# Optimization experiments

Hardware: AMD Instinct MI355X
Metric: run time of the kernel (lower is better)

The kernel has to match this reference:

```python
import jax, jax.numpy as jnp
import numpy as np

B, S, D = 4, 2048, 1024
E, H, K = 32, 128, 2


def setup_inputs() -> dict:
    key = jax.random.key(0)
    k1, k2, k3, k4 = jax.random.split(key, 4)
    scale_d = 1.0 / np.sqrt(D)
    scale_h = 1.0 / np.sqrt(H)
    return {
        "x": jax.random.normal(k1, (B, S, D), dtype=jnp.float32),
        "w_sel": jax.random.normal(k2, (E, D), dtype=jnp.float32) * scale_d,      # router Linear weight [E, D]
        "w_keys": jax.random.normal(k3, (E, D, H), dtype=jnp.float32) * scale_d,  # per-expert up-proj
        "w_values": jax.random.normal(k4, (E, H, D), dtype=jnp.float32) * scale_h, # per-expert down-proj
        "k": K,
    }


def reference(x, w_sel, w_keys, w_values, k):
    # Router: sigmoid gating + top-k expert selection per token.
    sel = jax.nn.sigmoid(jnp.einsum('bsd,ed->bse', x, w_sel))      # [B,S,E]
    sel_val, sel_idx = jax.lax.top_k(sel, k)                       # [B,S,k]
    n_exp = w_sel.shape[0]
    # Dense gate matrix: gate[b,s,e] = sum of sel_val over heads routed to e
    # (top_k indices are distinct, so this matches the per-head accumulation).
    gate = jnp.sum(jax.nn.one_hot(sel_idx, n_exp, dtype=x.dtype) * sel_val[..., None], axis=-2)  # [B,S,E]
    # Expert up-projection + ReLU for all experts (dense equivalent of the
    # per-token gathered keys[expert_idx](token); unselected experts are
    # zeroed by the gate so the math is identical).
    scores = jax.nn.relu(jnp.einsum('bsd,edh->bseh', x, w_keys))   # [B,S,E,H]
    weighted = scores * gate[..., None]                            # [B,S,E,H]
    out = jnp.einsum('bseh,ehd->bsd', weighted, w_values)          # [B,S,D]
    return out
```

## Files before the change

### kernel.cpp

```cpp
#include <hip/hip_runtime.h>
#include <cstdint>
#include <cstddef>

#define NTOK 8192
#define DIM  1024
#define NEXP 32
#define NH   128
#define TT   64
#define FTILES 16
#define BK   128
#define RT   32
#define LCAP 1024

typedef __attribute__((ext_vector_type(8))) short short8;
typedef __attribute__((ext_vector_type(4))) float float4_;

static __device__ __forceinline__ unsigned short f2bf(float f) {
  unsigned u = __float_as_uint(f);
  return (unsigned short)((u + 0x7fffu + ((u >> 16) & 1u)) >> 16);
}
static __device__ __forceinline__ float bf2f(unsigned short h) {
  return __uint_as_float(((unsigned)h) << 16);
}
static __device__ __forceinline__ void gload_lds16(const unsigned short* g,
                                                   unsigned short* l) {
  __builtin_amdgcn_global_load_lds(
      (const __attribute__((address_space(1))) unsigned int*)(const void*)g,
      (__attribute__((address_space(3))) unsigned int*)(void*)l, 16, 0, 0);
}

__global__ __launch_bounds__(256) void prep_kernel(
    const float* __restrict__ w_keys, const float* __restrict__ w_values,
    const float* __restrict__ x,
    unsigned short* __restrict__ wk_t, unsigned short* __restrict__ wv_t,
    unsigned short* __restrict__ xbf, int* __restrict__ counts)
{
  __shared__ float tile[32][33];
  const int bid = blockIdx.x;
  const int tid = threadIdx.x;
  if (bid == 0 && tid < NEXP) counts[tid] = 0;

  if (bid < 8192) {
    const float* src; unsigned short* dst; int R, C, lb;
    if (bid < 4096) { src = w_keys;   dst = wk_t; R = DIM; C = NH;  lb = bid; }
    else            { src = w_values; dst = wv_t; R = NH;  C = DIM; lb = bid - 4096; }
    const int e  = lb >> 7;
    const int t  = lb & 127;
    const int tpc = C >> 5;
    const int r0 = (t / tpc) * 32;
    const int c0 = (t % tpc) * 32;
    const float* s = src + (size_t)e * R * C;
    unsigned short* d = dst + (size_t)e * R * C;

    const int i = tid >> 3;
    const int j = (tid & 7) * 4;
    float4 v = *(const float4*)(s + (size_t)(r0 + i) * C + c0 + j);
    tile[i][j] = v.x; tile[i][j + 1] = v.y; tile[i][j + 2] = v.z; tile[i][j + 3] = v.w;
    __syncthreads();
    unsigned lo = (unsigned)f2bf(tile[j + 0][i]) | ((unsigned)f2bf(tile[j + 1][i]) << 16);
    unsigned hi = (unsigned)f2bf(tile[j + 2][i]) | ((unsigned)f2bf(tile[j + 3][i]) << 16);
    uint2 u; u.x = lo; u.y = hi;
    *(uint2*)(d + (size_t)(c0 + i) * R + r0 + j) = u;
  } else {
    const int lb = bid - 8192;
    size_t i = ((size_t)lb * 256 + tid) * 8;
    float4 a = *(const float4*)(x + i);
    float4 b = *(const float4*)(x + i + 4);
    uint4 u;
    u.x = (unsigned)f2bf(a.x) | ((unsigned)f2bf(a.y) << 16);
    u.y = (unsigned)f2bf(a.z) | ((unsigned)f2bf(a.w) << 16);
    u.z = (unsigned)f2bf(b.x) | ((unsigned)f2bf(b.y) << 16);
    u.w = (unsigned)f2bf(b.z) | ((unsigned)f2bf(b.w) << 16);
    *(uint4*)(xbf + i) = u;
  }
}

__global__ __launch_bounds__(256) void router_kernel(
    const float* __restrict__ x, const float* __restrict__ w_sel,
    int* __restrict__ counts, unsigned* __restrict__ list)
{
  __shared__ __align__(16) float xs_t[64][36];
  __shared__ float ws[NEXP][65];
  __shared__ float S[RT][33];

  const int tid  = threadIdx.x;
  const int tok0 = blockIdx.x * RT;
  const int tr   = tid >> 3;
  const int d8   = (tid & 7) * 8;
  const int tg4  = (tid & 7) * 4;

  float acc[4] = {0.f, 0.f, 0.f, 0.f};

  for (int dc = 0; dc < DIM; dc += 64) {
    const float* xp = x + (size_t)(tok0 + tr) * DIM + dc + d8;
    float4 a0 = *(const float4*)(xp);
    float4 a1 = *(const float4*)(xp + 4);
    xs_t[d8 + 0][tr] = a0.x; xs_t[d8 + 1][tr] = a0.y;
    xs_t[d8 + 2][tr] = a0.z; xs_t[d8 + 3][tr] = a0.w;
    xs_t[d8 + 4][tr] = a1.x; xs_t[d8 + 5][tr] = a1.y;
    xs_t[d8 + 6][tr] = a1.z; xs_t[d8 + 7][tr] = a1.w;
    const float* wp = w_sel + (size_t)tr * DIM + dc + d8;
    float4 b0 = *(const float4*)(wp);
    float4 b1 = *(const float4*)(wp + 4);
    ws[tr][d8 + 0] = b0.x; ws[tr][d8 + 1] = b0.y;
    ws[tr][d8 + 2] = b0.z; ws[tr][d8 + 3] = b0.w;
    ws[tr][d8 + 4] = b1.x; ws[tr][d8 + 5] = b1.y;
    ws[tr][d8 + 6] = b1.z; ws[tr][d8 + 7] = b1.w;
    __syncthreads();

    #pragma unroll 8
    for (int d = 0; d < 64; ++d) {
      float w = ws[tr][d];
      float4 xv = *(const float4*)&xs_t[d][tg4];
      acc[0] += xv.x * w; acc[1] += xv.y * w;
      acc[2] += xv.z * w; acc[3] += xv.w * w;
    }
    __syncthreads();
  }

  #pragma unroll
  for (int j = 0; j < 4; ++j)
    S[tg4 + j][tr] = acc[j];
  __syncthreads();

  if (tid < RT) {
    const int t = tid;
    float m1 = -1e30f, m2 = -1e30f;
    int i1 = 0, i2 = 0;
    for (int ee = 0; ee < NEXP; ++ee) {
      float v = S[t][ee];
      if (v > m1)      { m2 = m1; i2 = i1; m1 = v; i1 = ee; }
      else if (v > m2) { m2 = v; i2 = ee; }
    }
    const int token = tok0 + t;
    float g1 = 1.f / (1.f + __expf(-m1));
    float g2 = 1.f / (1.f + __expf(-m2));
    unsigned e1 = ((unsigned)f2bf(g1) << 16) | ((unsigned)token << 1);
    unsigned e2 = ((unsigned)f2bf(g2) << 16) | ((unsigned)token << 1) | 1u;
    int p1 = atomicAdd(&counts[i1], 1);
    if (p1 < LCAP) list[i1 * LCAP + p1] = e1;
    int p2 = atomicAdd(&counts[i2], 1);
    if (p2 < LCAP) list[i2 * LCAP + p2] = e2;
  }
}

__global__ __launch_bounds__(256, 2) void ffn_kernel(
    const unsigned short* __restrict__ xbf,
    const unsigned short* __restrict__ wk_t,
    const unsigned short* __restrict__ wv_t,
    float* __restrict__ out,
    unsigned short* __restrict__ cont,
    const int* __restrict__ counts, const unsigned* __restrict__ list,
    int use_cont)
{
  const int bid = blockIdx.x;
  const int e   = bid & 31;
  const int cnt = min(counts[e], LCAP);

  __shared__ unsigned short xsf[2][16 * 512];
  __shared__ unsigned short ss[TT][NH + 8];
  __shared__ int   toks[TT];
  __shared__ float gates[TT];

  const int tid  = threadIdx.x;
  const int wave = tid >> 6;
  const int lane = tid & 63;
  const int quad = lane >> 4;
  const int l16  = lane & 15;

  const unsigned short* wkb = wk_t + (size_t)e * NH * DIM;
  const unsigned short* wvb = wv_t + (size_t)e * DIM * NH;

  for (int t0 = (bid >> 5) * TT; t0 < cnt; t0 += FTILES * TT) {
    const int n_tok = min(TT, cnt - t0);

    if (tid < TT) {
      int valid = tid < n_tok;
      unsigned en = valid ? list[e * LCAP + t0 + tid] : 0u;
      toks[tid]  = valid ? (int)(en & 0xffffu) : -1;
      gates[tid] = valid ? bf2f((unsigned short)(en >> 16)) : 0.f;
    }
    __syncthreads();

    int slot = toks[wave * 16 + l16];
    int gtok = (slot < 0) ? 0 : (slot >> 1);
    const unsigned short* gsrc = xbf + (size_t)gtok * DIM + quad * 8;

    #pragma unroll
    for (int kk = 0; kk < 4; ++kk)
      gload_lds16(gsrc + kk * 32, &xsf[0][(wave * 4 + kk) * 512]);
    __syncthreads();

    float4_ acc[4][2];
    #pragma unroll
    for (int mt = 0; mt < 4; ++mt)
      #pragma unroll
      for (int nt = 0; nt < 2; ++nt) acc[mt][nt] = (float4_){0.f, 0.f, 0.f, 0.f};

    for (int ci = 0; ci < 8; ++ci) {
      const int dc = ci * BK;
      if (ci < 7) {
        const int nb = (ci + 1) & 1;
        #pragma unroll
        for (int kk = 0; kk < 4; ++kk)
          gload_lds16(gsrc + dc + BK + kk * 32, &xsf[nb][(wave * 4 + kk) * 512]);
      }
      short8 b[4][2];
      #pragma unroll
      for (int kk = 0; kk < 4; ++kk)
        #pragma unroll
        for (int nt = 0; nt < 2; ++nt)
          b[kk][nt] = *(const short8*)(wkb +
              (size_t)(wave * 32 + nt * 16 + l16) * DIM + dc + kk * 32 + quad * 8);

      const unsigned short* xb = &xsf[ci & 1][0];
      #pragma unroll
      for (int kk = 0; kk < 4; ++kk) {
        #pragma unroll
        for (int mt = 0; mt < 4; ++mt) {
          short8 a = *(const short8*)(xb + (mt * 4 + kk) * 512 + lane * 8);
          #pragma unroll
          for (int nt = 0; nt < 2; ++nt)
            acc[mt][nt] = __builtin_amdgcn_mfma_f32_16x16x32_bf16(a, b[kk][nt], acc[mt][nt], 0, 0, 0);
        }
      }
      __syncthreads();
    }

    #pragma unroll
    for (int mt = 0; mt < 4; ++mt)
      #pragma unroll
      for (int nt = 0; nt < 2; ++nt)
        #pragma unroll
        for (int r = 0; r < 4; ++r) {
          int row = mt * 16 + quad * 4 + r;
          float v = fmaxf(acc[mt][nt][r], 0.f) * gates[row];
          ss[row][wave * 32 + nt * 16 + l16] = f2bf(v);
        }
    __syncthreads();

    #pragma unroll 1
    for (int nc = 0; nc < 4; ++nc) {
      const int colbase = wave * 256 + nc * 64;
      float4_ o[4][4];
      #pragma unroll
      for (int mt = 0; mt < 4; ++mt)
        #pragma unroll
        for (int nt = 0; nt < 4; ++nt) o[mt][nt] = (float4_){0.f, 0.f, 0.f, 0.f};

      short8 b2[4][4];
      #pragma unroll
      for (int kk = 0; kk < 4; ++kk)
        #pragma unroll
        for (int nt = 0; nt < 4; ++nt)
          b2[kk][nt] = *(const short8*)(wvb +
              (size_t)(colbase + nt * 16 + l16) * NH + kk * 32 + quad * 8);

      #pragma unroll
      for (int kk = 0; kk < 4; ++kk) {
        short8 a[4];
        #pragma unroll
        for (int mt = 0; mt < 4; ++mt)
          a[mt] = *(const short8*)&ss[mt * 16 + l16][kk * 32 + quad * 8];
        #pragma unroll
        for (int mt = 0; mt < 4; ++mt)
          #pragma unroll
          for (int nt = 0; nt < 4; ++nt)
            o[mt][nt] = __builtin_amdgcn_mfma_f32_16x16x32_bf16(a[mt], b2[kk][nt], o[mt][nt], 0, 0, 0);
      }

      if (use_cont) {
        #pragma unroll
        for (int mt = 0; mt < 4; ++mt)
          #pragma unroll
          for (int r = 0; r < 4; ++r) {
            int row = mt * 16 + quad * 4 + r;
            if (row < n_tok) {
              int sl = toks[row];
              size_t base = ((size_t)((sl & 1) * NTOK + (sl >> 1))) * DIM + colbase;
              #pragma unroll
              for (int nt = 0; nt < 4; ++nt)
                cont[base + nt * 16 + l16] = f2bf(o[mt][nt][r]);
            }
          }
      } else {
        #pragma unroll
        for (int mt = 0; mt < 4; ++mt)
          #pragma unroll
          for (int r = 0; r < 4; ++r) {
            int row = mt * 16 + quad * 4 + r;
            if (row < n_tok) {
              size_t base = (size_t)(toks[row] >> 1) * DIM + colbase;
              #pragma unroll
              for (int nt = 0; nt < 4; ++nt)
                unsafeAtomicAdd(&out[base + nt * 16 + l16], o[mt][nt][r]);
            }
          }
      }
    }
    __syncthreads();
  }
}

__global__ __launch_bounds__(256) void combine_kernel(
    const unsigned short* __restrict__ cont, float* __restrict__ out)
{
  size_t i = ((size_t)blockIdx.x * 256 + threadIdx.x) * 8;
  uint4 a = *(const uint4*)(cont + i);
  uint4 b = *(const uint4*)(cont + (size_t)NTOK * DIM + i);
  float4 r0, r1;
  r0.x = bf2f((unsigned short)(a.x & 0xffff)) + bf2f((unsigned short)(b.x & 0xffff));
  r0.y = bf2f((unsigned short)(a.x >> 16))    + bf2f((unsigned short)(b.x >> 16));
  r0.z = bf2f((unsigned short)(a.y & 0xffff)) + bf2f((unsigned short)(b.y & 0xffff));
  r0.w = bf2f((unsigned short)(a.y >> 16))    + bf2f((unsigned short)(b.y >> 16));
  r1.x = bf2f((unsigned short)(a.z & 0xffff)) + bf2f((unsigned short)(b.z & 0xffff));
  r1.y = bf2f((unsigned short)(a.z >> 16))    + bf2f((unsigned short)(b.z >> 16));
  r1.z = bf2f((unsigned short)(a.w & 0xffff)) + bf2f((unsigned short)(b.w & 0xffff));
  r1.w = bf2f((unsigned short)(a.w >> 16))    + bf2f((unsigned short)(b.w >> 16));
  *(float4*)(out + i) = r0;
  *(float4*)(out + i + 4) = r1;
}

extern "C" void kernel_launch(void* const* d_in, const int* in_sizes, int n_in,
                              void* d_out, int out_size, void* d_ws, size_t ws_size,
                              hipStream_t stream) {
  (void)in_sizes; (void)n_in;
  const float* x        = (const float*)d_in[0];
  const float* w_sel    = (const float*)d_in[1];
  const float* w_keys   = (const float*)d_in[2];
  const float* w_values = (const float*)d_in[3];
  float* out = (float*)d_out;

  char* ws = (char*)d_ws;
  size_t off = 0;
  int*            counts = (int*)(ws + off);            off += 4096;
  unsigned*       list   = (unsigned*)(ws + off);       off += (size_t)NEXP * LCAP * 4;
  unsigned short* wk_t   = (unsigned short*)(ws + off); off += (size_t)NEXP * NH * DIM * 2;
  unsigned short* wv_t   = (unsigned short*)(ws + off); off += (size_t)NEXP * NH * DIM * 2;
  unsigned short* xbf    = (unsigned short*)(ws + off); off += (size_t)NTOK * DIM * 2;
  unsigned short* cont   = (unsigned short*)(ws + off);
  size_t need_full = off + (size_t)2 * NTOK * DIM * 2;
  const int use_cont = (ws_size >= need_full) ? 1 : 0;

  prep_kernel<<<12288, 256, 0, stream>>>(w_keys, w_values, x, wk_t, wv_t, xbf, counts);

  router_kernel<<<NTOK / RT, 256, 0, stream>>>(x, w_sel, counts, list);

  if (!use_cont)
    hipMemsetAsync(out, 0, (size_t)out_size * sizeof(float), stream);

  ffn_kernel<<<NEXP * FTILES, 256, 0, stream>>>(xbf, wk_t, wv_t, out, cont,
                                                counts, list, use_cont);

  if (use_cont)
    combine_kernel<<<NTOK * DIM / (256 * 8), 256, 0, stream>>>(cont, out);
}
```

Baseline: 249.8 us.

## Split expert FFN into two choice passes and fuse router into prep kernel

Routing lists are now kept per (expert, top-k slot), and the FFN runs as two passes. The first pass writes output rows directly and the second adds into them, which removes the bf16 contribution buffer, the combine kernel and the atomics. The router is merged into the prep kernel launch, and the FFN is retiled to 32 tokens with the D dimension split in halves. The up-projection now reads operands straight from global memory instead of staging them through LDS. The change also lowers the per-list capacity to 512, which risks silently dropping tokens if routing is imbalanced, and the router inside prep reads x while other blocks of the same launch convert it.

Result: slower. 336.2 us (+34.6%).

```diff
diff --git a/kernel.cpp b/kernel.cpp
--- a/kernel.cpp
+++ b/kernel.cpp
@@ -6,13 +6,13 @@
 #define DIM  1024
 #define NEXP 32
 #define NH   128
-#define TT   64
-#define FTILES 16
-#define BK   128
+#define TT   32
+#define SLOTS 16
+#define LCAP2 512
 #define RT   32
-#define LCAP 1024
 
 typedef __attribute__((ext_vector_type(8))) short short8;
+typedef __attribute__((ext_vector_type(4))) short short4_;
 typedef __attribute__((ext_vector_type(4))) float float4_;
 
 static __device__ __forceinline__ unsigned short f2bf(float f) {
@@ -22,23 +22,21 @@
 static __device__ __forceinline__ float bf2f(unsigned short h) {
   return __uint_as_float(((unsigned)h) << 16);
 }
-static __device__ __forceinline__ void gload_lds16(const unsigned short* g,
-                                                   unsigned short* l) {
-  __builtin_amdgcn_global_load_lds(
-      (const __attribute__((address_space(1))) unsigned int*)(const void*)g,
-      (__attribute__((address_space(3))) unsigned int*)(void*)l, 16, 0, 0);
-}
-
-__global__ __launch_bounds__(256) void prep_kernel(
+
+__global__ __launch_bounds__(256) void prep_router_kernel(
     const float* __restrict__ w_keys, const float* __restrict__ w_values,
-    const float* __restrict__ x,
+    const float* __restrict__ x, const float* __restrict__ w_sel,
     unsigned short* __restrict__ wk_t, unsigned short* __restrict__ wv_t,
-    unsigned short* __restrict__ xbf, int* __restrict__ counts)
+    unsigned short* __restrict__ xbf,
+    int* __restrict__ counts, unsigned* __restrict__ list)
 {
   __shared__ float tile[32][33];
+  __shared__ __align__(16) float xs_t[64][36];
+  __shared__ float ws[NEXP][65];
+  __shared__ float S[RT][33];
+
   const int bid = blockIdx.x;
   const int tid = threadIdx.x;
-  if (bid == 0 && tid < NEXP) counts[tid] = 0;
 
   if (bid < 8192) {
     const float* src; unsigned short* dst; int R, C, lb;
@@ -61,7 +59,7 @@
     unsigned hi = (unsigned)f2bf(tile[j + 2][i]) | ((unsigned)f2bf(tile[j + 3][i]) << 16);
     uint2 u; u.x = lo; u.y = hi;
     *(uint2*)(d + (size_t)(c0 + i) * R + r0 + j) = u;
-  } else {
+  } else if (bid < 12288) {
     const int lb = bid - 8192;
     size_t i = ((size_t)lb * 256 + tid) * 8;
     float4 a = *(const float4*)(x + i);
@@ -72,93 +70,81 @@
     u.z = (unsigned)f2bf(b.x) | ((unsigned)f2bf(b.y) << 16);
     u.w = (unsigned)f2bf(b.z) | ((unsigned)f2bf(b.w) << 16);
     *(uint4*)(xbf + i) = u;
+  } else {
+    const int tok0 = (bid - 12288) * RT;
+    const int tr   = tid >> 3;
+    const int d8   = (tid & 7) * 8;
+    const int tg4  = (tid & 7) * 4;
+
+    float acc[4] = {0.f, 0.f, 0.f, 0.f};
+
+    for (int dc = 0; dc < DIM; dc += 64) {
+      const float* xp = x + (size_t)(tok0 + tr) * DIM + dc + d8;
+      float4 a0 = *(const float4*)(xp);
+      float4 a1 = *(const float4*)(xp + 4);
+      xs_t[d8 + 0][tr] = a0.x; xs_t[d8 + 1][tr] = a0.y;
+      xs_t[d8 + 2][tr] = a0.z; xs_t[d8 + 3][tr] = a0.w;
+      xs_t[d8 + 4][tr] = a1.x; xs_t[d8 + 5][tr] = a1.y;
+      xs_t[d8 + 6][tr] = a1.z; xs_t[d8 + 7][tr] = a1.w;
+      const float* wp = w_sel + (size_t)tr * DIM + dc + d8;
+      float4 b0 = *(const float4*)(wp);
+      float4 b1 = *(const float4*)(wp + 4);
+      ws[tr][d8 + 0] = b0.x; ws[tr][d8 + 1] = b0.y;
+      ws[tr][d8 + 2] = b0.z; ws[tr][d8 + 3] = b0.w;
+      ws[tr][d8 + 4] = b1.x; ws[tr][d8 + 5] = b1.y;
+      ws[tr][d8 + 6] = b1.z; ws[tr][d8 + 7] = b1.w;
+      __syncthreads();
+
+      #pragma unroll 8
+      for (int d = 0; d < 64; ++d) {
+        float w = ws[tr][d];
+        float4 xv = *(const float4*)&xs_t[d][tg4];
+        acc[0] += xv.x * w; acc[1] += xv.y * w;
+        acc[2] += xv.z * w; acc[3] += xv.w * w;
+      }
+      __syncthreads();
+    }
+
+    #pragma unroll
+    for (int j = 0; j < 4; ++j)
+      S[tg4 + j][tr] = acc[j];
+    __syncthreads();
+
+    if (tid < RT) {
+      const int t = tid;
+      float m1 = -1e30f, m2 = -1e30f;
+      int i1 = 0, i2 = 0;
+      for (int ee = 0; ee < NEXP; ++ee) {
+        float v = S[t][ee];
+        if (v > m1)      { m2 = m1; i2 = i1; m1 = v; i1 = ee; }
+        else if (v > m2) { m2 = v; i2 = ee; }
+      }
+      const int token = tok0 + t;
+      float g1 = 1.f / (1.f + __expf(-m1));
+      float g2 = 1.f / (1.f + __expf(-m2));
+      int p1 = atomicAdd(&counts[i1 * 2 + 0], 1);
+      if (p1 < LCAP2) list[(i1 * 2 + 0) * LCAP2 + p1] = ((unsigned)f2bf(g1) << 16) | (unsigned)token;
+      int p2 = atomicAdd(&counts[i2 * 2 + 1], 1);
+      if (p2 < LCAP2) list[(i2 * 2 + 1) * LCAP2 + p2] = ((unsigned)f2bf(g2) << 16) | (unsigned)token;
+    }
   }
 }
 
-__global__ __launch_bounds__(256) void router_kernel(
-    const float* __restrict__ x, const float* __restrict__ w_sel,
-    int* __restrict__ counts, unsigned* __restrict__ list)
-{
-  __shared__ __align__(16) float xs_t[64][36];
-  __shared__ float ws[NEXP][65];
-  __shared__ float S[RT][33];
-
-  const int tid  = threadIdx.x;
-  const int tok0 = blockIdx.x * RT;
-  const int tr   = tid >> 3;
-  const int d8   = (tid & 7) * 8;
-  const int tg4  = (tid & 7) * 4;
-
-  float acc[4] = {0.f, 0.f, 0.f, 0.f};
-
-  for (int dc = 0; dc < DIM; dc += 64) {
-    const float* xp = x + (size_t)(tok0 + tr) * DIM + dc + d8;
-    float4 a0 = *(const float4*)(xp);
-    float4 a1 = *(const float4*)(xp + 4);
-    xs_t[d8 + 0][tr] = a0.x; xs_t[d8 + 1][tr] = a0.y;
-    xs_t[d8 + 2][tr] = a0.z; xs_t[d8 + 3][tr] = a0.w;
-    xs_t[d8 + 4][tr] = a1.x; xs_t[d8 + 5][tr] = a1.y;
-    xs_t[d8 + 6][tr] = a1.z; xs_t[d8 + 7][tr] = a1.w;
-    const float* wp = w_sel + (size_t)tr * DIM + dc + d8;
-    float4 b0 = *(const float4*)(wp);
-    float4 b1 = *(const float4*)(wp + 4);
-    ws[tr][d8 + 0] = b0.x; ws[tr][d8 + 1] = b0.y;
-    ws[tr][d8 + 2] = b0.z; ws[tr][d8 + 3] = b0.w;
-    ws[tr][d8 + 4] = b1.x; ws[tr][d8 + 5] = b1.y;
-    ws[tr][d8 + 6] = b1.z; ws[tr][d8 + 7] = b1.w;
-    __syncthreads();
-
-    #pragma unroll 8
-    for (int d = 0; d < 64; ++d) {
-      float w = ws[tr][d];
-      float4 xv = *(const float4*)&xs_t[d][tg4];
-      acc[0] += xv.x * w; acc[1] += xv.y * w;
-      acc[2] += xv.z * w; acc[3] += xv.w * w;
-    }
-    __syncthreads();
-  }
-
-  #pragma unroll
-  for (int j = 0; j < 4; ++j)
-    S[tg4 + j][tr] = acc[j];
-  __syncthreads();
-
-  if (tid < RT) {
-    const int t = tid;
-    float m1 = -1e30f, m2 = -1e30f;
-    int i1 = 0, i2 = 0;
-    for (int ee = 0; ee < NEXP; ++ee) {
-      float v = S[t][ee];
-      if (v > m1)      { m2 = m1; i2 = i1; m1 = v; i1 = ee; }
-      else if (v > m2) { m2 = v; i2 = ee; }
-    }
-    const int token = tok0 + t;
-    float g1 = 1.f / (1.f + __expf(-m1));
-    float g2 = 1.f / (1.f + __expf(-m2));
-    unsigned e1 = ((unsigned)f2bf(g1) << 16) | ((unsigned)token << 1);
-    unsigned e2 = ((unsigned)f2bf(g2) << 16) | ((unsigned)token << 1) | 1u;
-    int p1 = atomicAdd(&counts[i1], 1);
-    if (p1 < LCAP) list[i1 * LCAP + p1] = e1;
-    int p2 = atomicAdd(&counts[i2], 1);
-    if (p2 < LCAP) list[i2 * LCAP + p2] = e2;
-  }
-}
-
-__global__ __launch_bounds__(256, 2) void ffn_kernel(
+__global__ __launch_bounds__(256, 2) void ffn_pass_kernel(
     const unsigned short* __restrict__ xbf,
     const unsigned short* __restrict__ wk_t,
     const unsigned short* __restrict__ wv_t,
     float* __restrict__ out,
-    unsigned short* __restrict__ cont,
     const int* __restrict__ counts, const unsigned* __restrict__ list,
-    int use_cont)
+    int choice)
 {
-  const int bid = blockIdx.x;
-  const int e   = bid & 31;
-  const int cnt = min(counts[e], LCAP);
-
-  __shared__ unsigned short xsf[2][16 * 512];
-  __shared__ unsigned short ss[TT][NH + 8];
+  const int bid   = blockIdx.x;
+  const int e     = bid & 31;
+  const int dhalf = (bid >> 5) & 1;
+  const int slot  = bid >> 6;
+  const int cnt   = min(counts[e * 2 + choice], LCAP2);
+
+  __shared__ __align__(16) unsigned short ss2[16][TT][8];
   __shared__ int   toks[TT];
   __shared__ float gates[TT];
 
@@ -170,161 +156,105 @@
 
   const unsigned short* wkb = wk_t + (size_t)e * NH * DIM;
   const unsigned short* wvb = wv_t + (size_t)e * DIM * NH;
-
-  for (int t0 = (bid >> 5) * TT; t0 < cnt; t0 += FTILES * TT) {
+  const unsigned* lst = list + (size_t)(e * 2 + choice) * LCAP2;
+
+  for (int t0 = slot * TT; t0 < cnt; t0 += SLOTS * TT) {
     const int n_tok = min(TT, cnt - t0);
-
+    __syncthreads();
     if (tid < TT) {
       int valid = tid < n_tok;
-      unsigned en = valid ? list[e * LCAP + t0 + tid] : 0u;
-      toks[tid]  = valid ? (int)(en & 0xffffu) : -1;
+      unsigned en = valid ? lst[t0 + tid] : 0u;
+      toks[tid]  = (int)(en & 0xffffu);
       gates[tid] = valid ? bf2f((unsigned short)(en >> 16)) : 0.f;
     }
     __syncthreads();
 
-    int slot = toks[wave * 16 + l16];
-    int gtok = (slot < 0) ? 0 : (slot >> 1);
-    const unsigned short* gsrc = xbf + (size_t)gtok * DIM + quad * 8;
-
-    #pragma unroll
-    for (int kk = 0; kk < 4; ++kk)
-      gload_lds16(gsrc + kk * 32, &xsf[0][(wave * 4 + kk) * 512]);
-    __syncthreads();
-
-    float4_ acc[4][2];
-    #pragma unroll
-    for (int mt = 0; mt < 4; ++mt)
-      #pragma unroll
-      for (int nt = 0; nt < 2; ++nt) acc[mt][nt] = (float4_){0.f, 0.f, 0.f, 0.f};
-
-    for (int ci = 0; ci < 8; ++ci) {
-      const int dc = ci * BK;
-      if (ci < 7) {
-        const int nb = (ci + 1) & 1;
+    const unsigned short* xg0 = xbf + (size_t)toks[l16]      * DIM + quad * 8;
+    const unsigned short* xg1 = xbf + (size_t)toks[16 + l16] * DIM + quad * 8;
+    const unsigned short* wg0 = wkb + (size_t)((wave * 2 + 0) * 16 + l16) * DIM + quad * 8;
+    const unsigned short* wg1 = wkb + (size_t)((wave * 2 + 1) * 16 + l16) * DIM + quad * 8;
+
+    float4_ accA[2][2];
+    #pragma unroll
+    for (int i = 0; i < 2; ++i)
+      #pragma unroll
+      for (int j = 0; j < 2; ++j) accA[i][j] = (float4_){0.f, 0.f, 0.f, 0.f};
+
+    #pragma unroll 8
+    for (int ks = 0; ks < 32; ++ks) {
+      const int off = ks * 32;
+      short8 a0 = *(const short8*)(wg0 + off);
+      short8 a1 = *(const short8*)(wg1 + off);
+      short8 b0 = *(const short8*)(xg0 + off);
+      short8 b1 = *(const short8*)(xg1 + off);
+      accA[0][0] = __builtin_amdgcn_mfma_f32_16x16x32_bf16(a0, b0, accA[0][0], 0, 0, 0);
+      accA[0][1] = __builtin_amdgcn_mfma_f32_16x16x32_bf16(a0, b1, accA[0][1], 0, 0, 0);
+      accA[1][0] = __builtin_amdgcn_mfma_f32_16x16x32_bf16(a1, b0, accA[1][0], 0, 0, 0);
+      accA[1][1] = __builtin_amdgcn_mfma_f32_16x16x32_bf16(a1, b1, accA[1][1], 0, 0, 0);
+    }
+
+    #pragma unroll
+    for (int ht = 0; ht < 2; ++ht) {
+      const int hb = (wave * 2 + ht) * 2 + (quad >> 1);
+      #pragma unroll
+      for (int tt = 0; tt < 2; ++tt) {
+        const int t = tt * 16 + l16;
+        const float g = gates[t];
+        short4_ w;
         #pragma unroll
-        for (int kk = 0; kk < 4; ++kk)
-          gload_lds16(gsrc + dc + BK + kk * 32, &xsf[nb][(wave * 4 + kk) * 512]);
-      }
-      short8 b[4][2];
-      #pragma unroll
-      for (int kk = 0; kk < 4; ++kk)
+        for (int r = 0; r < 4; ++r)
+          w[r] = (short)f2bf(fmaxf(accA[ht][tt][r], 0.f) * g);
+        *(short4_*)&ss2[hb][t][(quad & 1) * 4] = w;
+      }
+    }
+    __syncthreads();
+
+    float4_ accB[8][2];
+    #pragma unroll
+    for (int i = 0; i < 8; ++i)
+      #pragma unroll
+      for (int j = 0; j < 2; ++j) accB[i][j] = (float4_){0.f, 0.f, 0.f, 0.f};
+
+    #pragma unroll
+    for (int ks = 0; ks < 4; ++ks) {
+      short8 b0 = *(const short8*)&ss2[ks * 4 + quad][l16][0];
+      short8 b1 = *(const short8*)&ss2[ks * 4 + quad][16 + l16][0];
+      #pragma unroll
+      for (int i = 0; i < 8; ++i) {
+        const int d = (dhalf * 32 + wave * 8 + i) * 16 + l16;
+        short8 a = *(const short8*)(wvb + (size_t)d * NH + ks * 32 + quad * 8);
+        accB[i][0] = __builtin_amdgcn_mfma_f32_16x16x32_bf16(a, b0, accB[i][0], 0, 0, 0);
+        accB[i][1] = __builtin_amdgcn_mfma_f32_16x16x32_bf16(a, b1, accB[i][1], 0, 0, 0);
+      }
+    }
+
+    #pragma unroll
+    for (int tt = 0; tt < 2; ++tt) {
+      const int t = tt * 16 + l16;
+      if (t < n_tok) {
+        float* rowp = out + (size_t)toks[t] * DIM +
+                      (dhalf * 32 + wave * 8) * 16 + quad * 4;
         #pragma unroll
-        for (int nt = 0; nt < 2; ++nt)
-          b[kk][nt] = *(const short8*)(wkb +
-              (size_t)(wave * 32 + nt * 16 + l16) * DIM + dc + kk * 32 + quad * 8);
-
-      const unsigned short* xb = &xsf[ci & 1][0];
-      #pragma unroll
-      for (int kk = 0; kk < 4; ++kk) {
-        #pragma unroll
-        for (int mt = 0; mt < 4; ++mt) {
-          short8 a = *(const short8*)(xb + (mt * 4 + kk) * 512 + lane * 8);
-          #pragma unroll
-          for (int nt = 0; nt < 2; ++nt)
-            acc[mt][nt] = __builtin_amdgcn_mfma_f32_16x16x32_bf16(a, b[kk][nt], acc[mt][nt], 0, 0, 0);
+        for (int i = 0; i < 8; ++i) {
+          float4 v;
+          v.x = accB[i][tt][0]; v.y = accB[i][tt][1];
+          v.z = accB[i][tt][2]; v.w = accB[i][tt][3];
+          float* p = rowp + i * 16;
+          if (choice) {
+            float4 o = *(float4*)p;
+            v.x += o.x; v.y += o.y; v.z += o.z; v.w += o.w;
+          }
+          *(float4*)p = v;
         }
       }
-      __syncthreads();
-    }
-
-    #pragma unroll
-    for (int mt = 0; mt < 4; ++mt)
-      #pragma unroll
-      for (int nt = 0; nt < 2; ++nt)
-        #pragma unroll
-        for (int r = 0; r < 4; ++r) {
-          int row = mt * 16 + quad * 4 + r;
-          float v = fmaxf(acc[mt][nt][r], 0.f) * gates[row];
-          ss[row][wave * 32 + nt * 16 + l16] = f2bf(v);
-        }
-    __syncthreads();
-
-    #pragma unroll 1
-    for (int nc = 0; nc < 4; ++nc) {
-      const int colbase = wave * 256 + nc * 64;
-      float4_ o[4][4];
-      #pragma unroll
-      for (int mt = 0; mt < 4; ++mt)
-        #pragma unroll
-        for (int nt = 0; nt < 4; ++nt) o[mt][nt] = (float4_){0.f, 0.f, 0.f, 0.f};
-
-      short8 b2[4][4];
-      #pragma unroll
-      for (int kk = 0; kk < 4; ++kk)
-        #pragma unroll
-        for (int nt = 0; nt < 4; ++nt)
-          b2[kk][nt] = *(const short8*)(wvb +
-              (size_t)(colbase + nt * 16 + l16) * NH + kk * 32 + quad * 8);
-
-      #pragma unroll
-      for (int kk = 0; kk < 4; ++kk) {
-        short8 a[4];
-        #pragma unroll
-        for (int mt = 0; mt < 4; ++mt)
-          a[mt] = *(const short8*)&ss[mt * 16 + l16][kk * 32 + quad * 8];
-        #pragma unroll
-        for (int mt = 0; mt < 4; ++mt)
-          #pragma unroll
-          for (int nt = 0; nt < 4; ++nt)
-            o[mt][nt] = __builtin_amdgcn_mfma_f32_16x16x32_bf16(a[mt], b2[kk][nt], o[mt][nt], 0, 0, 0);
-      }
-
-      if (use_cont) {
-        #pragma unroll
-        for (int mt = 0; mt < 4; ++mt)
-          #pragma unroll
-          for (int r = 0; r < 4; ++r) {
-            int row = mt * 16 + quad * 4 + r;
-            if (row < n_tok) {
-              int sl = toks[row];
-              size_t base = ((size_t)((sl & 1) * NTOK + (sl >> 1))) * DIM + colbase;
-              #pragma unroll
-              for (int nt = 0; nt < 4; ++nt)
-                cont[base + nt * 16 + l16] = f2bf(o[mt][nt][r]);
-            }
-          }
-      } else {
-        #pragma unroll
-        for (int mt = 0; mt < 4; ++mt)
-          #pragma unroll
-          for (int r = 0; r < 4; ++r) {
-            int row = mt * 16 + quad * 4 + r;
-            if (row < n_tok) {
-              size_t base = (size_t)(toks[row] >> 1) * DIM + colbase;
-              #pragma unroll
-              for (int nt = 0; nt < 4; ++nt)
-                unsafeAtomicAdd(&out[base + nt * 16 + l16], o[mt][nt][r]);
-            }
-          }
-      }
-    }
-    __syncthreads();
+    }
   }
-}
-
-__global__ __launch_bounds__(256) void combine_kernel(
-    const unsigned short* __restrict__ cont, float* __restrict__ out)
-{
-  size_t i = ((size_t)blockIdx.x * 256 + threadIdx.x) * 8;
-  uint4 a = *(const uint4*)(cont + i);
-  uint4 b = *(const uint4*)(cont + (size_t)NTOK * DIM + i);
-  float4 r0, r1;
-  r0.x = bf2f((unsigned short)(a.x & 0xffff)) + bf2f((unsigned short)(b.x & 0xffff));
-  r0.y = bf2f((unsigned short)(a.x >> 16))    + bf2f((unsigned short)(b.x >> 16));
-  r0.z = bf2f((unsigned short)(a.y & 0xffff)) + bf2f((unsigned short)(b.y & 0xffff));
-  r0.w = bf2f((unsigned short)(a.y >> 16))    + bf2f((unsigned short)(b.y >> 16));
-  r1.x = bf2f((unsigned short)(a.z & 0xffff)) + bf2f((unsigned short)(b.z & 0xffff));
-  r1.y = bf2f((unsigned short)(a.z >> 16))    + bf2f((unsigned short)(b.z >> 16));
-  r1.z = bf2f((unsigned short)(a.w & 0xffff)) + bf2f((unsigned short)(b.w & 0xffff));
-  r1.w = bf2f((unsigned short)(a.w >> 16))    + bf2f((unsigned short)(b.w >> 16));
-  *(float4*)(out + i) = r0;
-  *(float4*)(out + i + 4) = r1;
 }
 
 extern "C" void kernel_launch(void* const* d_in, const int* in_sizes, int n_in,
                               void* d_out, int out_size, void* d_ws, size_t ws_size,
                               hipStream_t stream) {
-  (void)in_sizes; (void)n_in;
+  (void)in_sizes; (void)n_in; (void)ws_size; (void)out_size;
   const float* x        = (const float*)d_in[0];
   const float* w_sel    = (const float*)d_in[1];
   const float* w_keys   = (const float*)d_in[2];
@@ -334,24 +264,18 @@
   char* ws = (char*)d_ws;
   size_t off = 0;
   int*            counts = (int*)(ws + off);            off += 4096;
-  unsigned*       list   = (unsigned*)(ws + off);       off += (size_t)NEXP * LCAP * 4;
+  unsigned*       list   = (unsigned*)(ws + off);       off += (size_t)NEXP * 2 * LCAP2 * 4;
   unsigned short* wk_t   = (unsigned short*)(ws + off); off += (size_t)NEXP * NH * DIM * 2;
   unsigned short* wv_t   = (unsigned short*)(ws + off); off += (size_t)NEXP * NH * DIM * 2;
-  unsigned short* xbf    = (unsigned short*)(ws + off); off += (size_t)NTOK * DIM * 2;
-  unsigned short* cont   = (unsigned short*)(ws + off);
-  size_t need_full = off + (size_t)2 * NTOK * DIM * 2;
-  const int use_cont = (ws_size >= need_full) ? 1 : 0;
-
-  prep_kernel<<<12288, 256, 0, stream>>>(w_keys, w_values, x, wk_t, wv_t, xbf, counts);
-
-  router_kernel<<<NTOK / RT, 256, 0, stream>>>(x, w_sel, counts, list);
-
-  if (!use_cont)
-    hipMemsetAsync(out, 0, (size_t)out_size * sizeof(float), stream);
-
-  ffn_kernel<<<NEXP * FTILES, 256, 0, stream>>>(xbf, wk_t, wv_t, out, cont,
-                                                counts, list, use_cont);
-
-  if (use_cont)
-    combine_kernel<<<NTOK * DIM / (256 * 8), 256, 0, stream>>>(cont, out);
-}
+  unsigned short* xbf    = (unsigned short*)(ws + off);
+
+  hipMemsetAsync(counts, 0, sizeof(int) * NEXP * 2, stream);
+
+  prep_router_kernel<<<12544, 256, 0, stream>>>(w_keys, w_values, x, w_sel,
+                                                wk_t, wv_t, xbf, counts, list);
+
+  ffn_pass_kernel<<<NEXP * 2 * SLOTS, 256, 0, stream>>>(
+      xbf, wk_t, wv_t, out, counts, list, 0);
+  ffn_pass_kernel<<<NEXP * 2 * SLOTS, 256, 0, stream>>>(
+      xbf, wk_t, wv_t, out, counts, list, 1);
+}
```
